# Optimization experiments

Measured on AMD Instinct MI355X. Metric: run time of the kernel, lower is better.

Reference implementation:

```python
import jax, jax.numpy as jnp
import numpy as np

NUM_BITS = 4
BLOCK = 64
OUT_F, IN_F = 4096, 4096
RANK = 16


def _uniform_table():
    # BlockQuantizer.create_uniform_map(symmetric=False, num_bits=4)
    return jnp.linspace(-1.0, 1.0, 2 ** NUM_BITS).astype(jnp.float32)


def _dequantize(qweight, weight_max):
    """Unpack 4-bit codes (2 per byte), lookup codebook, apply per-64 block scale.
    qweight: [OUT*IN/2, 1] int32 in [0,256); weight_max: [OUT*IN/64, 1] float32.
    Returns [OUT_F, IN_F] float32."""
    table = _uniform_table()
    q = qweight[:, 0]
    idx_lo = q & 15          # packed at shift 0
    idx_hi = (q >> 4) & 15   # packed at shift 4
    w = jnp.stack([table[idx_lo], table[idx_hi]], axis=-1)  # [N/2, 2]
    w = w.reshape(-1, BLOCK) * weight_max                   # per-block scale
    return w.reshape(OUT_F, IN_F)


def setup_inputs() -> dict:
    key = jax.random.key(0)
    k1, k2, k3, k4, k5, k6 = jax.random.split(key, 6)
    x = jax.random.normal(k1, (4, 2048, IN_F), dtype=jnp.float32)
    qweight = jax.random.randint(k2, (OUT_F * IN_F // 2, 1), 0, 256, dtype=jnp.int32)
    weight_max = jax.random.uniform(k3, (OUT_F * IN_F // BLOCK, 1), dtype=jnp.float32,
                                    minval=0.01, maxval=1.0)
    lora_A = jax.random.normal(k4, (RANK, IN_F), dtype=jnp.float32) * 0.02
    lora_B = jax.random.normal(k5, (OUT_F, RANK), dtype=jnp.float32) * 0.02
    bias = jax.random.normal(k6, (OUT_F,), dtype=jnp.float32) * 0.02
    return {"x": x, "qweight": qweight, "weight_max": weight_max,
            "lora_A": lora_A, "lora_B": lora_B, "bias": bias}


def reference(x, qweight, weight_max, lora_A, lora_B, bias):
    # Dequantize block-quantized base weight, then linear + LoRA correction.
    W = _dequantize(qweight, weight_max)                     # [out, in]
    y = jnp.einsum('bsi,oi->bso', x, W) + bias               # base linear
    a = jnp.einsum('bsi,ri->bsr', x, lora_A)                 # lora_A(x)
    y = y + jnp.einsum('bsr,or->bso', a, lora_B)             # + lora_B(.)
    return y
```

## Files before the change

kernel.cpp:

```cpp
#include <hip/hip_runtime.h>
#include <hip/hip_bf16.h>
#include <stdint.h>

typedef __bf16 bf16_t;
typedef bf16_t bf16x8 __attribute__((ext_vector_type(8)));
typedef float f32x4 __attribute__((ext_vector_type(4)));

#define IN_F 4096
#define OUT_F 4096
#define M_ROWS 8192
#define RANK 16

__global__ __launch_bounds__(256)
void prep_kernel(const float* __restrict__ x, const int* __restrict__ qw,
                 const float* __restrict__ wmax, const float* __restrict__ lA,
                 const float* __restrict__ lB, bf16_t* __restrict__ Wp,
                 bf16_t* __restrict__ Xb) {
  const int b = blockIdx.x;
  if (b >= 8192) {
    const size_t tid = (size_t)(b - 8192) * 256 + threadIdx.x;
    const float4 a0 = *(const float4*)(x + tid * 8);
    const float4 a1 = *(const float4*)(x + tid * 8 + 4);
    bf16x8 o;
    o[0] = (bf16_t)a0.x; o[1] = (bf16_t)a0.y; o[2] = (bf16_t)a0.z; o[3] = (bf16_t)a0.w;
    o[4] = (bf16_t)a1.x; o[5] = (bf16_t)a1.y; o[6] = (bf16_t)a1.z; o[7] = (bf16_t)a1.w;
    *(bf16x8*)(Xb + tid * 8) = o;
    return;
  }
  const int bo = b >> 4;
  const int bi = b & 15;
  const int t  = threadIdx.x;
  const int o  = bo * 8 + (t >> 5);
  const int i0 = bi * 256 + (t & 31) * 8;
  const int f0 = o * IN_F + i0;

  const int4 q4 = *(const int4*)(qw + (f0 >> 1));
  const float scale = wmax[f0 >> 6];
  const float st = scale * (2.0f / 15.0f);

  float v[8];
  {
    const int q0 = q4.x, q1 = q4.y, q2 = q4.z, q3 = q4.w;
    v[0] = (float)(q0 & 15)        * st - scale;
    v[1] = (float)((q0 >> 4) & 15) * st - scale;
    v[2] = (float)(q1 & 15)        * st - scale;
    v[3] = (float)((q1 >> 4) & 15) * st - scale;
    v[4] = (float)(q2 & 15)        * st - scale;
    v[5] = (float)((q2 >> 4) & 15) * st - scale;
    v[6] = (float)(q3 & 15)        * st - scale;
    v[7] = (float)((q3 >> 4) & 15) * st - scale;
  }

  const float* Brow = lB + o * RANK;
#pragma unroll
  for (int r = 0; r < RANK; ++r) {
    const float br = Brow[r];
    const float4 a0 = *(const float4*)(lA + r * IN_F + i0);
    const float4 a1 = *(const float4*)(lA + r * IN_F + i0 + 4);
    v[0] += br * a0.x; v[1] += br * a0.y; v[2] += br * a0.z; v[3] += br * a0.w;
    v[4] += br * a1.x; v[5] += br * a1.y; v[6] += br * a1.z; v[7] += br * a1.w;
  }

  bf16x8 ov;
#pragma unroll
  for (int j = 0; j < 8; ++j) ov[j] = (bf16_t)v[j];
  *(bf16x8*)(Wp + (size_t)f0) = ov;
}

__device__ __forceinline__ void gld(const bf16_t* src, char* dst) {
  __builtin_amdgcn_global_load_lds((const __attribute__((address_space(1))) void*)src,
                                   (__attribute__((address_space(3))) void*)dst, 16, 0, 0);
}

#define BARRIER() __builtin_amdgcn_s_barrier()
#define WAIT_LGKM0() do { asm volatile("s_waitcnt lgkmcnt(0)" ::: "memory"); \
                          __builtin_amdgcn_sched_barrier(0); } while (0)
#define WAIT_VM(n) asm volatile("s_waitcnt vmcnt(" #n ")" ::: "memory")

#define STAGE(kt, buf) do { \
  gld(Asrc + (size_t)(kt) * 32,                      ldsA + (buf)*8192  + tid*16); \
  gld(Bsrc + (size_t)(kt) * 32,                      ldsB + (buf)*16384 + tid*16); \
  gld(Bsrc + (size_t)128*IN_F + (size_t)(kt) * 32,   ldsB + (buf)*16384 + 8192 + tid*16); \
} while (0)

#define LDAf(buf, m) (*(const bf16x8*)(ldsA + (buf)*8192  + aRowB + (m)*1024 + cSw))
#define LDBf(buf, n) (*(const bf16x8*)(ldsB + (buf)*16384 + bRowB + (n)*1024 + cSw))

#define TILE(CUR, STG, TW) do { \
  _Pragma("unroll") for (int m = 0; m < 4; ++m) a[m] = LDAf(CUR, m); \
  _Pragma("unroll") for (int n = 0; n < 4; ++n) b[n] = LDBf(CUR, n); \
  WAIT_LGKM0(); \
  BARRIER(); \
  STG; \
  __builtin_amdgcn_s_setprio(1); \
  _Pragma("unroll") for (int m = 0; m < 4; ++m) \
  _Pragma("unroll") for (int n = 0; n < 4; ++n) \
    acc[m][n] = __builtin_amdgcn_mfma_f32_16x16x32_bf16(a[m], b[n], acc[m][n], 0, 0, 0); \
  __builtin_amdgcn_s_setprio(0); \
  TW; \
  BARRIER(); \
} while (0)

__global__ __launch_bounds__(512, 4)
void gemm_occ2_kernel(const bf16_t* __restrict__ Xb, const bf16_t* __restrict__ Wp,
                      const float* __restrict__ bias, float* __restrict__ C) {
  __shared__ __align__(16) bf16_t As[2 * 4096];
  __shared__ __align__(16) bf16_t Bs[2 * 8192];
  char* ldsA = (char*)As;
  char* ldsB = (char*)Bs;

  const int tid  = threadIdx.x;
  const int lane = tid & 63;
  const int wave = tid >> 6;
  const int wr = wave >> 2;
  const int wc = wave & 3;
  const int r16 = lane & 15;
  const int kg  = lane >> 4;

  const int bid  = blockIdx.x;
  const int wgid = (bid & 7) * 128 + (bid >> 3);
  const int bm = wgid >> 4;
  const int bn = wgid & 15;

  const int srow = tid >> 2;
  const int ss   = (tid & 3) ^ ((tid >> 3) & 3);
  const bf16_t* Asrc = Xb + (size_t)(bm * 128 + srow) * IN_F + ss * 8;
  const bf16_t* Bsrc = Wp + (size_t)(bn * 256 + srow) * IN_F + ss * 8;

  const int cSw   = (kg ^ ((r16 >> 1) & 3)) * 16;
  const int aRowB = (wr * 64 + r16) * 64;
  const int bRowB = (wc * 64 + r16) * 64;

  f32x4 acc[4][4] = {};
  bf16x8 a[4], b[4];

  STAGE(0, 0);
  STAGE(1, 1);
  WAIT_VM(3);
  BARRIER();

  for (int tt = 0; tt < 124; tt += 2) {
    TILE(0, STAGE(tt + 2, 0), WAIT_VM(3));
    TILE(1, STAGE(tt + 3, 1), WAIT_VM(3));
  }
  TILE(0, STAGE(126, 0), WAIT_VM(3));
  TILE(1, STAGE(127, 1), WAIT_VM(3));
  TILE(0, {},            WAIT_VM(0));
  TILE(1, {},            {});

#pragma unroll
  for (int n = 0; n < 4; ++n) {
    const int col = bn * 256 + wc * 64 + n * 16 + r16;
    const float bv = bias[col];
#pragma unroll
    for (int m = 0; m < 4; ++m) {
      const int row0 = bm * 128 + wr * 64 + m * 16 + kg * 4;
#pragma unroll
      for (int r = 0; r < 4; ++r)
        C[(size_t)(row0 + r) * OUT_F + col] = acc[m][n][r] + bv;
    }
  }
}

extern "C" void kernel_launch(void* const* d_in, const int* in_sizes, int n_in,
                              void* d_out, int out_size, void* d_ws, size_t ws_size,
                              hipStream_t stream) {
  const float* x  = (const float*)d_in[0];
  const int*   qw = (const int*)d_in[1];
  const float* wm = (const float*)d_in[2];
  const float* lA = (const float*)d_in[3];
  const float* lB = (const float*)d_in[4];
  const float* bs = (const float*)d_in[5];
  float* out = (float*)d_out;

  bf16_t* Wp = (bf16_t*)d_ws;
  bf16_t* Xb = (bf16_t*)((char*)d_ws + (size_t)OUT_F * IN_F * 2);

  prep_kernel<<<24576, 256, 0, stream>>>(x, qw, wm, lA, lB, Wp, Xb);
  gemm_occ2_kernel<<<(M_ROWS / 128) * (OUT_F / 256), 512, 0, stream>>>(Xb, Wp, bs, out);
}
```

Baseline: 334.5 us.

## Triple-buffer LDS and interleave register-prefetched LDS reads with MFMAs

Moves the GEMM main loop from double-buffered LDS to a three-stage ring and ping-pongs two register fragment sets. The LDS reads for the next tile are interleaved with the MFMAs on the current tile, and the barrier plus lgkmcnt wait that sat before each compute phase are dropped. This is meant to hide LDS read latency and cut barrier stalls per k-step. In exchange it uses more LDS and registers, drops the occupancy hint in launch_bounds, and makes the buffer-index bookkeeping more intricate.

```diff
diff --git a/kernel.cpp b/kernel.cpp
--- a/kernel.cpp
+++ b/kernel.cpp
@@ -73,8 +73,6 @@
 }
 
 #define BARRIER() __builtin_amdgcn_s_barrier()
-#define WAIT_LGKM0() do { asm volatile("s_waitcnt lgkmcnt(0)" ::: "memory"); \
-                          __builtin_amdgcn_sched_barrier(0); } while (0)
 #define WAIT_VM(n) asm volatile("s_waitcnt vmcnt(" #n ")" ::: "memory")
 
 #define STAGE(kt, buf) do { \
@@ -86,26 +84,29 @@
 #define LDAf(buf, m) (*(const bf16x8*)(ldsA + (buf)*8192  + aRowB + (m)*1024 + cSw))
 #define LDBf(buf, n) (*(const bf16x8*)(ldsB + (buf)*16384 + bRowB + (n)*1024 + cSw))
 
-#define TILE(CUR, STG, TW) do { \
-  _Pragma("unroll") for (int m = 0; m < 4; ++m) a[m] = LDAf(CUR, m); \
-  _Pragma("unroll") for (int n = 0; n < 4; ++n) b[n] = LDBf(CUR, n); \
-  WAIT_LGKM0(); \
-  BARRIER(); \
-  STG; \
-  __builtin_amdgcn_s_setprio(1); \
-  _Pragma("unroll") for (int m = 0; m < 4; ++m) \
+#define MFMA4(m, AB, BB) do { \
   _Pragma("unroll") for (int n = 0; n < 4; ++n) \
-    acc[m][n] = __builtin_amdgcn_mfma_f32_16x16x32_bf16(a[m], b[n], acc[m][n], 0, 0, 0); \
-  __builtin_amdgcn_s_setprio(0); \
-  TW; \
-  BARRIER(); \
+    acc[m][n] = __builtin_amdgcn_mfma_f32_16x16x32_bf16(AB[m], BB[n], acc[m][n], 0, 0, 0); \
 } while (0)
 
-__global__ __launch_bounds__(512, 4)
-void gemm_occ2_kernel(const bf16_t* __restrict__ Xb, const bf16_t* __restrict__ Wp,
-                      const float* __restrict__ bias, float* __restrict__ C) {
-  __shared__ __align__(16) bf16_t As[2 * 4096];
-  __shared__ __align__(16) bf16_t Bs[2 * 8192];
+#define TILE(R, S, WA, WB, MA, MB, STG, VMW) do { \
+  VMW; BARRIER(); \
+  STG; \
+  WA[0] = LDAf(R, 0); WB[0] = LDBf(R, 0); \
+  MFMA4(0, MA, MB); \
+  WA[1] = LDAf(R, 1); WB[1] = LDBf(R, 1); \
+  MFMA4(1, MA, MB); \
+  WA[2] = LDAf(R, 2); WB[2] = LDBf(R, 2); \
+  MFMA4(2, MA, MB); \
+  WA[3] = LDAf(R, 3); WB[3] = LDBf(R, 3); \
+  MFMA4(3, MA, MB); \
+} while (0)
+
+__global__ __launch_bounds__(512)
+void gemm_ilv_kernel(const bf16_t* __restrict__ Xb, const bf16_t* __restrict__ Wp,
+                     const float* __restrict__ bias, float* __restrict__ C) {
+  __shared__ __align__(16) bf16_t As[3 * 4096];
+  __shared__ __align__(16) bf16_t Bs[3 * 8192];
   char* ldsA = (char*)As;
   char* ldsB = (char*)Bs;
 
@@ -132,21 +133,31 @@
   const int bRowB = (wc * 64 + r16) * 64;
 
   f32x4 acc[4][4] = {};
-  bf16x8 a[4], b[4];
+  bf16x8 eA[4], eB[4], oA[4], oB[4];
 
-  STAGE(0, 0);
-  STAGE(1, 1);
-  WAIT_VM(3);
+  STAGE(0, 0); STAGE(1, 1); STAGE(2, 2);
+  WAIT_VM(6);
   BARRIER();
+#pragma unroll
+  for (int m = 0; m < 4; ++m) { eA[m] = LDAf(0, m); eB[m] = LDBf(0, m); }
 
-  for (int tt = 0; tt < 124; tt += 2) {
-    TILE(0, STAGE(tt + 2, 0), WAIT_VM(3));
-    TILE(1, STAGE(tt + 3, 1), WAIT_VM(3));
+  for (int tt = 0; tt < 120; tt += 6) {
+    TILE(1, 0, oA, oB, eA, eB, STAGE(tt + 3, 0), WAIT_VM(3));
+    TILE(2, 1, eA, eB, oA, oB, STAGE(tt + 4, 1), WAIT_VM(3));
+    TILE(0, 2, oA, oB, eA, eB, STAGE(tt + 5, 2), WAIT_VM(3));
+    TILE(1, 0, eA, eB, oA, oB, STAGE(tt + 6, 0), WAIT_VM(3));
+    TILE(2, 1, oA, oB, eA, eB, STAGE(tt + 7, 1), WAIT_VM(3));
+    TILE(0, 2, eA, eB, oA, oB, STAGE(tt + 8, 2), WAIT_VM(3));
   }
-  TILE(0, STAGE(126, 0), WAIT_VM(3));
-  TILE(1, STAGE(127, 1), WAIT_VM(3));
-  TILE(0, {},            WAIT_VM(0));
-  TILE(1, {},            {});
+  TILE(1, 0, oA, oB, eA, eB, STAGE(123, 0), WAIT_VM(3));
+  TILE(2, 1, eA, eB, oA, oB, STAGE(124, 1), WAIT_VM(3));
+  TILE(0, 2, oA, oB, eA, eB, STAGE(125, 2), WAIT_VM(3));
+  TILE(1, 0, eA, eB, oA, oB, STAGE(126, 0), WAIT_VM(3));
+  TILE(2, 1, oA, oB, eA, eB, STAGE(127, 1), WAIT_VM(3));
+  TILE(0, 2, eA, eB, oA, oB, {},            WAIT_VM(3));
+  TILE(1, 2, oA, oB, eA, eB, {},            WAIT_VM(0));
+  { BARRIER();
+    MFMA4(0, oA, oB); MFMA4(1, oA, oB); MFMA4(2, oA, oB); MFMA4(3, oA, oB); }
 
 #pragma unroll
   for (int n = 0; n < 4; ++n) {
@@ -177,5 +188,5 @@
   bf16_t* Xb = (bf16_t*)((char*)d_ws + (size_t)OUT_F * IN_F * 2);
 
   prep_kernel<<<24576, 256, 0, stream>>>(x, qw, wm, lA, lB, Wp, Xb);
-  gemm_occ2_kernel<<<(M_ROWS / 128) * (OUT_F / 256), 512, 0, stream>>>(Xb, Wp, bs, out);
+  gemm_ilv_kernel<<<(M_ROWS / 128) * (OUT_F / 256), 512, 0, stream>>>(Xb, Wp, bs, out);
 }
```

New measurement: 377.7 us. 12.9% more time.
